# Performance work log

Hardware: AMD Instinct MI355X
Metric: run time of the kernel (lower is better)

## Reference

```python
import jax, jax.numpy as jnp
import numpy as np

B, H, W, DIM, WS, SHIFT, HEADS = 32, 56, 56, 256, 7, 3, 8
N = WS * WS          # 49 tokens per window
C2 = 2 * DIM         # concatenated two-modal channel dim
NW = (H // WS) * (W // WS)


def _rel_index(ws):
    coords = np.stack(np.meshgrid(np.arange(ws), np.arange(ws), indexing='ij')).reshape(2, -1)
    rel = (coords[:, :, None] - coords[:, None, :]).transpose(1, 2, 0)
    rel[:, :, 0] += ws - 1
    rel[:, :, 1] += ws - 1
    rel[:, :, 0] *= 2 * ws - 1
    return rel.sum(-1)  # (N, N) int

REL_IDX = _rel_index(WS).reshape(-1)


def _attn_mask():
    # standard Swin shifted-window mask: 0 / -100 per window pair
    img = np.zeros((H, W))
    cnt = 0
    for hs in (slice(0, H - WS), slice(H - WS, H - SHIFT), slice(H - SHIFT, H)):
        for ws_ in (slice(0, W - WS), slice(W - WS, W - SHIFT), slice(W - SHIFT, W)):
            img[hs, ws_] = cnt
            cnt += 1
    mw = img.reshape(H // WS, WS, W // WS, WS).transpose(0, 2, 1, 3).reshape(-1, N)
    d = mw[:, None, :] - mw[:, :, None]
    return np.where(d != 0, -100.0, 0.0).astype(np.float32)  # (nW, N, N)

ATTN_MASK = _attn_mask()


def _win_part(x):  # (B,H,W,C) -> (nW*B, N, C)
    b, c = x.shape[0], x.shape[-1]
    x = x.reshape(b, H // WS, WS, W // WS, WS, c).transpose(0, 1, 3, 2, 4, 5)
    return x.reshape(-1, N, c)


def _win_rev(w, b):  # (nW*B, N, C) -> (B,H,W,C)
    c = w.shape[-1]
    x = w.reshape(b, H // WS, W // WS, WS, WS, c).transpose(0, 1, 3, 2, 4, 5)
    return x.reshape(b, H, W, c)


def _ln(t, g, bb):
    m = t.mean(-1, keepdims=True)
    v = t.var(-1, keepdims=True)
    return (t - m) / jnp.sqrt(v + 1e-5) * g + bb


def setup_inputs() -> dict:
    key = jax.random.key(0)
    ks = jax.random.split(key, 8)
    def nrm(k, shape, s=0.02):
        return jax.random.normal(k, shape, jnp.float32) * s
    return {
        'x': jax.random.normal(ks[0], (B, H * W, DIM), jnp.float32),
        'y': jax.random.normal(ks[1], (B, H * W, DIM), jnp.float32),
        'g1': jnp.ones((DIM,), jnp.float32), 'b1': jnp.zeros((DIM,), jnp.float32),
        'rpb': nrm(ks[2], ((2 * WS - 1) * (2 * WS - 1), HEADS)),
        'w_qkv': nrm(ks[3], (6 * DIM, 2 * DIM)), 'b_qkv': jnp.zeros((6 * DIM,), jnp.float32),
        'w_proj': nrm(ks[4], (DIM, 2 * DIM)), 'b_proj': jnp.zeros((DIM,), jnp.float32),
        'g2': jnp.ones((DIM,), jnp.float32), 'b2': jnp.zeros((DIM,), jnp.float32),
        'w_fc1': nrm(ks[5], (4 * DIM, DIM)), 'b_fc1': jnp.zeros((4 * DIM,), jnp.float32),
        'w_fc2': nrm(ks[6], (DIM, 4 * DIM)), 'b_fc2': jnp.zeros((DIM,), jnp.float32),
    }


def reference(x, y, g1, b1, rpb, w_qkv, b_qkv, w_proj, b_proj, g2, b2, w_fc1, b_fc1, w_fc2, b_fc2):
    scale = (DIM // HEADS) ** -0.5  # as in __init__: head_dim = dim // num_heads
    shortcut = x
    xn = _ln(x, g1, b1).reshape(B, H, W, DIM)
    yn = _ln(y, g1, b1).reshape(B, H, W, DIM)
    # cyclic shift
    xn = jnp.roll(xn, (-SHIFT, -SHIFT), axis=(1, 2))
    yn = jnp.roll(yn, (-SHIFT, -SHIFT), axis=(1, 2))
    xw, yw = _win_part(xn), _win_part(yn)            # (nW*B, N, C)
    xy = jnp.concatenate([xw, yw], axis=-1)          # (nW*B, N, 2C)
    nwb, hd = xy.shape[0], C2 // HEADS
    qkv = (xy @ w_qkv.T + b_qkv).reshape(nwb, N, 3, HEADS, hd).transpose(2, 0, 3, 1, 4)
    q, k, v = qkv[0] * scale, qkv[1], qkv[2]         # (nW*B, h, N, d)
    attn = jnp.einsum('whnd,whmd->whnm', q, k)
    bias = rpb[REL_IDX].reshape(N, N, HEADS).transpose(2, 0, 1)  # (h, N, N)
    attn = attn + bias[None]
    attn = attn.reshape(B, NW, HEADS, N, N) + jnp.asarray(ATTN_MASK)[None, :, None]
    attn = jax.nn.softmax(attn.reshape(nwb, HEADS, N, N), axis=-1)
    out = jnp.einsum('whnm,whmd->whnd', attn, v).transpose(0, 2, 1, 3).reshape(nwb, N, C2)
    out = out @ w_proj.T + b_proj                    # fuse 2C -> C
    out = _win_rev(out, B)
    out = jnp.roll(out, (SHIFT, SHIFT), axis=(1, 2)).reshape(B, H * W, DIM)
    x = shortcut + out
    h = _ln(x, g2, b2)
    h = jax.nn.gelu(h @ w_fc1.T + b_fc1, approximate=False)
    return x + h @ w_fc2.T + b_fc2
```

## Files before the change

### kernel.cpp

```cpp
#include <hip/hip_runtime.h>
#include <hip/hip_bf16.h>

#define DEVI __device__ __forceinline__

typedef __attribute__((ext_vector_type(8))) short short8;
typedef __attribute__((ext_vector_type(4))) float f32x4;
typedef unsigned int u32;
typedef unsigned short u16;

typedef __attribute__((address_space(1))) const u32 gu32_t;
typedef __attribute__((address_space(3))) u32 lu32_t;

DEVI u16 f2bf(float f) {
  u32 u = __builtin_bit_cast(u32, f);
  u32 r = (u + 0x7fffu + ((u >> 16) & 1u)) >> 16;
  return (u16)r;
}

DEVI f32x4 mfma16(short8 a, short8 b, f32x4 c) {
  return __builtin_amdgcn_mfma_f32_16x16x32_bf16(a, b, c, 0, 0, 0);
}

DEVI void gload16(const void* g, void* l) {
  __builtin_amdgcn_global_load_lds((gu32_t*)g, (lu32_t*)l, 16, 0, 0);
}

#define CHUNK_ROWS 25088
#define PLANE ((size_t)CHUNK_ROWS * 64)
#define KOFF  ((size_t)8 * PLANE)
#define VOFF  ((size_t)16 * PLANE)

__global__ __launch_bounds__(256) void convk(const float* __restrict__ s, u16* __restrict__ d, int n4) {
  int i = blockIdx.x * 256 + threadIdx.x;
  if (i < n4) {
    const float4 v = ((const float4*)s)[i];
    ushort4 o;
    o.x = f2bf(v.x); o.y = f2bf(v.y); o.z = f2bf(v.z); o.w = f2bf(v.w);
    ((ushort4*)d)[i] = o;
  }
}

__global__ __launch_bounds__(256) void btab_build(const float* __restrict__ rpb, float* __restrict__ btab) {
  const int cls = blockIdx.x >> 3, h = blockIdx.x & 7;
  float* dst = btab + (size_t)(cls * 8 + h) * 4096;
  for (int e = threadIdx.x; e < 4096; e += 256) {
    const int n = e >> 6, m = e & 63;
    float v;
    if (m >= 49) {
      v = -1e30f;
    } else if (n >= 49) {
      v = 0.f;
    } else {
      const int r1 = n / 7, c1 = n - r1 * 7;
      const int r2 = m / 7, c2 = m - r2 * 7;
      const int rel = (r1 - r2 + 6) * 13 + (c1 - c2 + 6);
      v = rpb[rel * 8 + h];
      const int reg1 = ((cls & 1) ? (r1 < 4 ? 1 : 2) : 0) * 3 + ((cls & 2) ? (c1 < 4 ? 1 : 2) : 0);
      const int reg2 = ((cls & 1) ? (r2 < 4 ? 1 : 2) : 0) * 3 + ((cls & 2) ? (c2 < 4 ? 1 : 2) : 0);
      if (reg1 != reg2) v -= 100.f;
    }
    dst[e] = v;
  }
}

__global__ __launch_bounds__(256) void ln_gather(
    const float* __restrict__ x, const float* __restrict__ y,
    const float* __restrict__ g1, const float* __restrict__ b1,
    u16* __restrict__ XY, int rowbase)
{
  const int wv = threadIdx.x >> 6, lane = threadIdx.x & 63;
  const int rl = blockIdx.x * 4 + wv;
  const int row = rowbase + rl;
  const int w = row / 49, n = row - w * 49;
  const int b = w >> 6, win = w & 63, wh = win >> 3, ww = win & 7;
  const int r = n / 7, c = n - r * 7;
  int oh = wh * 7 + r + 3; if (oh >= 56) oh -= 56;
  int ow = ww * 7 + c + 3; if (ow >= 56) ow -= 56;
  const size_t po = ((size_t)b * 3136 + oh * 56 + ow) * 256;
  const float4 g1v = ((const float4*)g1)[lane];
  const float4 b1v = ((const float4*)b1)[lane];
  u16* orow = XY + (size_t)rl * 512;
  #pragma unroll
  for (int mod = 0; mod < 2; ++mod) {
    const float* src = (mod ? y : x) + po;
    const float4 v = ((const float4*)src)[lane];
    float s = v.x + v.y + v.z + v.w;
    #pragma unroll
    for (int off = 1; off < 64; off <<= 1) s += __shfl_xor(s, off);
    const float mean = s * (1.0f / 256.0f);
    const float d0 = v.x - mean, d1 = v.y - mean, d2 = v.z - mean, d3 = v.w - mean;
    float sq = d0 * d0 + d1 * d1 + d2 * d2 + d3 * d3;
    #pragma unroll
    for (int off = 1; off < 64; off <<= 1) sq += __shfl_xor(sq, off);
    const float rstd = rsqrtf(sq * (1.0f / 256.0f) + 1e-5f);
    ushort4 o;
    o.x = f2bf(d0 * rstd * g1v.x + b1v.x);
    o.y = f2bf(d1 * rstd * g1v.y + b1v.y);
    o.z = f2bf(d2 * rstd * g1v.z + b1v.z);
    o.w = f2bf(d3 * rstd * g1v.w + b1v.w);
    *(ushort4*)(orow + mod * 256 + lane * 4) = o;
  }
}

__global__ __launch_bounds__(256) void qkv_gemm(
    const u16* __restrict__ A, const u16* __restrict__ Bw,
    const float* __restrict__ bias, u16* __restrict__ Qo)
{
  __shared__ __align__(16) u16 sA[128 * 64];
  __shared__ __align__(16) u16 sB[128 * 64];
  const int nx = gridDim.x;
  const int nwg = nx * gridDim.y;
  const int orig = blockIdx.y * nx + blockIdx.x;
  const int sw = (orig & 7) * (nwg >> 3) + (orig >> 3);
  const int m0  = (sw / nx) * 128;
  const int nn0 = (sw % nx) * 128;
  const int tid = threadIdx.x;
  const int lane = tid & 63;
  const int wv = tid >> 6;
  const int wm = wv >> 1, wn = wv & 1;
  const int rq = lane & 15, kg = lane >> 4;
  f32x4 acc[4][4];
  #pragma unroll
  for (int i = 0; i < 4; ++i)
    #pragma unroll
    for (int j = 0; j < 4; ++j) acc[i][j] = f32x4{0,0,0,0};

  for (int kt = 0; kt < 8; ++kt) {
    if (kt) __syncthreads();
    #pragma unroll
    for (int i = 0; i < 4; ++i) {
      const int c = i * 256 + tid;
      gload16(A + (size_t)(m0 + (c >> 3)) * 512 + kt * 64 + (c & 7) * 8, sA + c * 8);
    }
    #pragma unroll
    for (int i = 0; i < 4; ++i) {
      const int c = i * 256 + tid;
      gload16(Bw + (size_t)(nn0 + (c >> 3)) * 512 + kt * 64 + (c & 7) * 8, sB + c * 8);
    }
    __syncthreads();
    #pragma unroll
    for (int k0 = 0; k0 < 2; ++k0) {
      short8 af[4], bf8[4];
      #pragma unroll
      for (int mt = 0; mt < 4; ++mt)
        af[mt] = *(const short8*)(sA + (wm * 64 + mt * 16 + rq) * 64 + k0 * 32 + kg * 8);
      #pragma unroll
      for (int nt = 0; nt < 4; ++nt)
        bf8[nt] = *(const short8*)(sB + (wn * 64 + nt * 16 + rq) * 64 + k0 * 32 + kg * 8);
      #pragma unroll
      for (int mt = 0; mt < 4; ++mt)
        #pragma unroll
        for (int nt = 0; nt < 4; ++nt)
          acc[mt][nt] = mfma16(af[mt], bf8[nt], acc[mt][nt]);
    }
  }
  #pragma unroll
  for (int mt = 0; mt < 4; ++mt) {
    #pragma unroll
    for (int nt = 0; nt < 4; ++nt) {
      const int col = nn0 + wn * 64 + nt * 16 + rq;
      const int t = col >> 9, rem = col & 511;
      const int h = rem >> 6, d = rem & 63;
      const float bc = bias[col];
      const float sc = (t == 0) ? 0.17677669529663687f : 1.0f;
      u16* bp = Qo + (size_t)(t * 8 + h) * PLANE + d;
      #pragma unroll
      for (int r = 0; r < 4; ++r) {
        const int row = m0 + wm * 64 + mt * 16 + kg * 4 + r;
        bp[(size_t)row * 64] = f2bf((acc[mt][nt][r] + bc) * sc);
      }
    }
  }
}

__global__ __launch_bounds__(256, 3) void attn3(
    const u16* __restrict__ qkv, const float* __restrict__ btab,
    u16* __restrict__ concat, int wbase)
{
  __shared__ __align__(16) u16 sP[4][3136];
  __shared__ __align__(16) u16 sVT[4][4608];

  const int tid = threadIdx.x;
  const int wv = tid >> 6, lane = tid & 63;
  const int rq = lane & 15, kg = lane >> 4;
  const int gw = blockIdx.x * 4 + wv;
  const int wl = gw >> 3, h = gw & 7;
  const int w = wbase + wl;
  const int win = w & 63, wh = win >> 3, ww = win & 7;
  const int cls = ((wh == 7) ? 1 : 0) | ((ww == 7) ? 2 : 0);
  const float* Tb = btab + (size_t)(cls * 8 + h) * 4096;
  u16* sPw = sP[wv];
  u16* sVw = sVT[wv];

  const u16* qbase = qkv + (size_t)h * PLANE + (size_t)wl * 49 * 64;
  const u16* kbase = qkv + KOFF + (size_t)h * PLANE + (size_t)wl * 49 * 64;
  const u16* vbase = qkv + VOFF + (size_t)h * PLANE + (size_t)wl * 49 * 64;

  short8 vreg[4][2];
  #pragma unroll
  for (int t = 0; t < 4; ++t)
    #pragma unroll
    for (int h2 = 0; h2 < 2; ++h2)
      vreg[t][h2] = *(const short8*)(vbase + (size_t)(16 * t + rq) * 64 + kg * 8 + h2 * 32);

  short8 ak[4][2];
  #pragma unroll
  for (int j = 0; j < 4; ++j) {
    const int rr = (16 * j + rq) > 48 ? 48 : (16 * j + rq);
    ak[j][0] = *(const short8*)(kbase + rr * 64 + kg * 8);
    ak[j][1] = *(const short8*)(kbase + rr * 64 + 32 + kg * 8);
  }
  f32x4 sacc[4][4];
  #pragma unroll
  for (int i = 0; i < 4; ++i)
    #pragma unroll
    for (int j = 0; j < 4; ++j) sacc[i][j] = f32x4{0,0,0,0};
  #pragma unroll
  for (int i = 0; i < 4; ++i) {
    const int rr = (16 * i + rq) > 48 ? 48 : (16 * i + rq);
    const short8 a0 = *(const short8*)(qbase + rr * 64 + kg * 8);
    const short8 a1 = *(const short8*)(qbase + rr * 64 + 32 + kg * 8);
    #pragma unroll
    for (int j = 0; j < 4; ++j) {
      sacc[i][j] = mfma16(a0, ak[j][0], sacc[i][j]);
      sacc[i][j] = mfma16(a1, ak[j][1], sacc[i][j]);
    }
  }

  #pragma unroll
  for (int t = 0; t < 4; ++t) {
    const int row = 16 * t + rq;
    #pragma unroll
    for (int h2 = 0; h2 < 2; ++h2) {
      const int c0 = kg * 8 + h2 * 32;
      #pragma unroll
      for (int j = 0; j < 8; ++j)
        sVw[(c0 + j) * 72 + (row ^ (kg << 4))] = (u16)vreg[t][h2][j];
    }
  }

  #pragma unroll
  for (int i = 0; i < 4; ++i) {
    #pragma unroll
    for (int r = 0; r < 4; ++r) {
      const int n = 16 * i + kg * 4 + r;
      const float* Trow = Tb + n * 64 + rq;
      float pv[4];
      #pragma unroll
      for (int j = 0; j < 4; ++j)
        pv[j] = sacc[i][j][r] + Trow[16 * j];
      float mx = fmaxf(fmaxf(pv[0], pv[1]), fmaxf(pv[2], pv[3]));
      #pragma unroll
      for (int off = 1; off < 16; off <<= 1) mx = fmaxf(mx, __shfl_xor(mx, off));
      float sm = 0.f;
      #pragma unroll
      for (int j = 0; j < 4; ++j) { const float e = __expf(pv[j] - mx); pv[j] = e; sm += e; }
      #pragma unroll
      for (int off = 1; off < 16; off <<= 1) sm += __shfl_xor(sm, off);
      const float inv = 1.0f / sm;
      if (n < 49) {
        #pragma unroll
        for (int j = 0; j < 4; ++j) {
          const int col = 16 * j + rq;
          sPw[n * 64 + (((col >> 3) ^ (n & 7)) << 3) + (col & 7)] = f2bf(pv[j] * inv);
        }
      }
    }
  }

  f32x4 oacc[4][4];
  #pragma unroll
  for (int i = 0; i < 4; ++i)
    #pragma unroll
    for (int j = 0; j < 4; ++j) oacc[i][j] = f32x4{0,0,0,0};
  #pragma unroll
  for (int m0v = 0; m0v < 2; ++m0v) {
    short8 av[4];
    #pragma unroll
    for (int ct = 0; ct < 4; ++ct) {
      const int col = ct * 16 + rq;
      const int s = (col >> 3) & 3;
      short8 vvv = *(const short8*)(sVw + col * 72 + ((m0v * 32 + kg * 8) ^ (s << 4)));
      if (m0v == 1) {
        if (kg == 3) {
          #pragma unroll
          for (int e = 0; e < 8; ++e) vvv[e] = 0;
        } else if (kg == 2) {
          #pragma unroll
          for (int e = 1; e < 8; ++e) vvv[e] = 0;
        }
      }
      av[ct] = vvv;
    }
    #pragma unroll
    for (int i = 0; i < 4; ++i) {
      const int rr = (16 * i + rq) > 48 ? 48 : (16 * i + rq);
      const int ch = (m0v * 4 + kg) ^ (rr & 7);
      const short8 pa = *(const short8*)(sPw + rr * 64 + ch * 8);
      #pragma unroll
      for (int ct = 0; ct < 4; ++ct)
        oacc[i][ct] = mfma16(pa, av[ct], oacc[i][ct]);
    }
  }

  __builtin_amdgcn_s_waitcnt(0);
  #pragma unroll
  for (int i = 0; i < 4; ++i)
    #pragma unroll
    for (int ct = 0; ct < 4; ++ct)
      #pragma unroll
      for (int r = 0; r < 4; ++r) {
        const int n = 16 * i + kg * 4 + r;
        if (n < 49) {
          const int col = ct * 16 + rq;
          sPw[n * 64 + (((col >> 3) ^ (n & 7)) << 3) + (col & 7)] = f2bf(oacc[i][ct][r]);
        }
      }
  u16* crow = concat + (size_t)(wl * 49) * 512 + h * 64;
  #pragma unroll
  for (int it = 0; it < 7; ++it) {
    const int c = it * 64 + lane;
    if (c < 392) {
      const int m = c >> 3, s = c & 7;
      const short8 vvv = *(const short8*)(sPw + m * 64 + ((s ^ (m & 7)) << 3));
      *(short8*)(crow + (size_t)m * 512 + s * 8) = vvv;
    }
  }
}

__global__ __launch_bounds__(256, 2) void projln(
    const u16* __restrict__ A, const u16* __restrict__ Bw,
    const float* __restrict__ bias, const float* __restrict__ x,
    const float* __restrict__ g2, const float* __restrict__ b2,
    float* __restrict__ out, u16* __restrict__ xn2, int rowbase)
{
  __shared__ __align__(16) u16 sA[128 * 64];
  __shared__ __align__(16) u16 sB[256 * 64];
  const int m0 = blockIdx.x * 128;
  const int tid = threadIdx.x;
  const int lane = tid & 63;
  const int wv = tid >> 6;
  const int rq = lane & 15, kg = lane >> 4;
  f32x4 acc[2][16];
  #pragma unroll
  for (int i = 0; i < 2; ++i)
    #pragma unroll
    for (int j = 0; j < 16; ++j) acc[i][j] = f32x4{0,0,0,0};

  for (int kt = 0; kt < 8; ++kt) {
    if (kt) __syncthreads();
    #pragma unroll
    for (int i = 0; i < 4; ++i) {
      const int c = i * 256 + tid;
      gload16(A + (size_t)(m0 + (c >> 3)) * 512 + kt * 64 + (c & 7) * 8, sA + c * 8);
    }
    #pragma unroll
    for (int i = 0; i < 8; ++i) {
      const int c = i * 256 + tid;
      gload16(Bw + (size_t)(c >> 3) * 512 + kt * 64 + (c & 7) * 8, sB + c * 8);
    }
    __syncthreads();
    #pragma unroll
    for (int k0 = 0; k0 < 2; ++k0) {
      short8 af[2];
      #pragma unroll
      for (int mt = 0; mt < 2; ++mt)
        af[mt] = *(const short8*)(sA + (wv * 32 + mt * 16 + rq) * 64 + k0 * 32 + kg * 8);
      #pragma unroll
      for (int nt = 0; nt < 16; ++nt) {
        const short8 bf8 = *(const short8*)(sB + (nt * 16 + rq) * 64 + k0 * 32 + kg * 8);
        #pragma unroll
        for (int mt = 0; mt < 2; ++mt)
          acc[mt][nt] = mfma16(af[mt], bf8, acc[mt][nt]);
      }
    }
  }

  float br[16], g2r[16], b2r[16];
  #pragma unroll
  for (int nt = 0; nt < 16; ++nt) {
    const int col = nt * 16 + rq;
    br[nt] = bias[col]; g2r[nt] = g2[col]; b2r[nt] = b2[col];
  }
  #pragma unroll
  for (int mt = 0; mt < 2; ++mt) {
    #pragma unroll
    for (int r = 0; r < 4; ++r) {
      const int row = m0 + wv * 32 + mt * 16 + kg * 4 + r;
      const u32 g = (u32)(rowbase + row);
      const u32 w = g / 49u; const u32 n = g - w * 49u;
      const int b = w >> 6, win = w & 63, wh = win >> 3, ww = win & 7;
      const u32 rr = n / 7u; const u32 cc = n - rr * 7u;
      int oh = wh * 7 + (int)rr + 3; if (oh >= 56) oh -= 56;
      int ow = ww * 7 + (int)cc + 3; if (ow >= 56) ow -= 56;
      const size_t po = ((size_t)b * 3136 + oh * 56 + ow) * 256;
      float vals[16];
      float s = 0.f;
      #pragma unroll
      for (int nt = 0; nt < 16; ++nt) {
        const float v = acc[mt][nt][r] + br[nt] + x[po + nt * 16 + rq];
        vals[nt] = v; s += v;
      }
      #pragma unroll
      for (int off = 1; off < 16; off <<= 1) s += __shfl_xor(s, off);
      const float mean = s * (1.0f / 256.0f);
      float sq = 0.f;
      #pragma unroll
      for (int nt = 0; nt < 16; ++nt) { const float d_ = vals[nt] - mean; sq += d_ * d_; }
      #pragma unroll
      for (int off = 1; off < 16; off <<= 1) sq += __shfl_xor(sq, off);
      const float rstd = rsqrtf(sq * (1.0f / 256.0f) + 1e-5f);
      #pragma unroll
      for (int nt = 0; nt < 16; ++nt) {
        const int col = nt * 16 + rq;
        out[po + col] = vals[nt];
        xn2[po + col] = f2bf((vals[nt] - mean) * rstd * g2r[nt] + b2r[nt]);
      }
    }
  }
}

template<int K, int NOUT, bool GELU>
__global__ __launch_bounds__(256) void mlp_gemm(
    const u16* __restrict__ A, const u16* __restrict__ Bw,
    const float* __restrict__ bias, u16* __restrict__ obf, float* __restrict__ ofr)
{
  __shared__ __align__(16) u16 sA[128 * 64];
  __shared__ __align__(16) u16 sB[128 * 64];
  const int nx = gridDim.x;
  const int nwg = nx * gridDim.y;
  const int orig = blockIdx.y * nx + blockIdx.x;
  const int sw = (orig & 7) * (nwg >> 3) + (orig >> 3);
  const int m0  = (sw / nx) * 128;
  const int nn0 = (sw % nx) * 128;
  const int tid = threadIdx.x;
  const int lane = tid & 63;
  const int wv = tid >> 6;
  const int wm = wv >> 1, wn = wv & 1;
  const int rq = lane & 15, kg = lane >> 4;
  f32x4 acc[4][4];
  #pragma unroll
  for (int i = 0; i < 4; ++i)
    #pragma unroll
    for (int j = 0; j < 4; ++j) acc[i][j] = f32x4{0,0,0,0};

  for (int kt = 0; kt < K / 64; ++kt) {
    if (kt) __syncthreads();
    #pragma unroll
    for (int i = 0; i < 4; ++i) {
      const int c = i * 256 + tid;
      gload16(A + (size_t)(m0 + (c >> 3)) * K + kt * 64 + (c & 7) * 8, sA + c * 8);
    }
    #pragma unroll
    for (int i = 0; i < 4; ++i) {
      const int c = i * 256 + tid;
      gload16(Bw + (size_t)(nn0 + (c >> 3)) * K + kt * 64 + (c & 7) * 8, sB + c * 8);
    }
    __syncthreads();
    #pragma unroll
    for (int k0 = 0; k0 < 2; ++k0) {
      short8 af[4], bf8[4];
      #pragma unroll
      for (int mt = 0; mt < 4; ++mt)
        af[mt] = *(const short8*)(sA + (wm * 64 + mt * 16 + rq) * 64 + k0 * 32 + kg * 8);
      #pragma unroll
      for (int nt = 0; nt < 4; ++nt)
        bf8[nt] = *(const short8*)(sB + (wn * 64 + nt * 16 + rq) * 64 + k0 * 32 + kg * 8);
      #pragma unroll
      for (int mt = 0; mt < 4; ++mt)
        #pragma unroll
        for (int nt = 0; nt < 4; ++nt)
          acc[mt][nt] = mfma16(af[mt], bf8[nt], acc[mt][nt]);
    }
  }
  #pragma unroll
  for (int mt = 0; mt < 4; ++mt) {
    #pragma unroll
    for (int nt = 0; nt < 4; ++nt) {
      const int col = nn0 + wn * 64 + nt * 16 + rq;
      const float bcol = bias[col];
      #pragma unroll
      for (int r = 0; r < 4; ++r) {
        const int row = m0 + wm * 64 + mt * 16 + kg * 4 + r;
        float v = acc[mt][nt][r] + bcol;
        if constexpr (GELU) {
          v = 0.5f * v * (1.0f + erff(v * 0.7071067811865476f));
          obf[(size_t)row * NOUT + col] = f2bf(v);
        } else {
          float* p = ofr + (size_t)row * NOUT + col;
          *p = v + *p;
        }
      }
    }
  }
}

extern "C" void kernel_launch(void* const* d_in, const int* in_sizes, int n_in,
                              void* d_out, int out_size, void* d_ws, size_t ws_size,
                              hipStream_t stream) {
  const float* x      = (const float*)d_in[0];
  const float* y      = (const float*)d_in[1];
  const float* g1     = (const float*)d_in[2];
  const float* b1     = (const float*)d_in[3];
  const float* rpb    = (const float*)d_in[4];
  const float* w_qkv  = (const float*)d_in[5];
  const float* b_qkv  = (const float*)d_in[6];
  const float* w_proj = (const float*)d_in[7];
  const float* b_proj = (const float*)d_in[8];
  const float* g2     = (const float*)d_in[9];
  const float* b2     = (const float*)d_in[10];
  const float* w_fc1  = (const float*)d_in[11];
  const float* b_fc1  = (const float*)d_in[12];
  const float* w_fc2  = (const float*)d_in[13];
  const float* b_fc2  = (const float*)d_in[14];
  float* out = (float*)d_out;

  u16* wsp = (u16*)d_ws;
  u16* wqkv_bf  = wsp;
  u16* wproj_bf = wsp + 786432;
  u16* wfc1_bf  = wsp + 917504;
  u16* wfc2_bf  = wsp + 1179648;
  float* btab   = (float*)(wsp + 1441792);
  u16* xn2      = wsp + 1703936;
  u16* XYc      = wsp + 27394048;
  u16* qkvc     = wsp + 40239104;
  u16* hbuf     = XYc;

  convk<<<768, 256, 0, stream>>>(w_qkv,  wqkv_bf,  196608);
  convk<<<128, 256, 0, stream>>>(w_proj, wproj_bf, 32768);
  convk<<<256, 256, 0, stream>>>(w_fc1,  wfc1_bf,  65536);
  convk<<<256, 256, 0, stream>>>(w_fc2,  wfc2_bf,  65536);
  btab_build<<<32, 256, 0, stream>>>(rpb, btab);

  for (int c = 0; c < 4; ++c) {
    ln_gather<<<6272, 256, 0, stream>>>(x, y, g1, b1, XYc, c * CHUNK_ROWS);
    qkv_gemm<<<dim3(12, 196), 256, 0, stream>>>(XYc, wqkv_bf, b_qkv, qkvc);
    attn3<<<1024, 256, 0, stream>>>(qkvc, btab, XYc, c * 512);
    projln<<<196, 256, 0, stream>>>(XYc, wproj_bf, b_proj, x, g2, b2, out, xn2, c * CHUNK_ROWS);
  }

  for (int c = 0; c < 2; ++c) {
    mlp_gemm<256, 1024, true><<<dim3(8, 392), 256, 0, stream>>>(
        xn2 + (size_t)c * 50176 * 256, wfc1_bf, b_fc1, hbuf, nullptr);
    mlp_gemm<1024, 256, false><<<dim3(2, 392), 256, 0, stream>>>(
        hbuf, wfc2_bf, b_fc2, nullptr, out + (size_t)c * 50176 * 256);
  }
}
```

Before: 964.6 us.

## Fuse MLP fc1, GELU and fc2 into one kernel with the hidden tile kept in LDS

Replaces the two chunked MLP GEMM launches with a single kernel. Each block takes 64 rows, stages the LayerNorm output in XOR-swizzled LDS, and builds the hidden layer 128 columns at a time. Each hidden slice goes through GELU into LDS and is immediately accumulated into the fc2 result, so the 1024-wide hidden activation is never written to or read back from global memory. Weight fragments are read straight from global memory/cache rather than staged in LDS, which may cost bandwidth. The exact erf GELU is also replaced with a tanh approximation using __expf, which slightly changes the numerics relative to the reference.

Result: faster. 866.2 us (-10.2%).

```diff
diff --git a/kernel.cpp b/kernel.cpp
--- a/kernel.cpp
+++ b/kernel.cpp
@@ -23,6 +23,12 @@
 
 DEVI void gload16(const void* g, void* l) {
   __builtin_amdgcn_global_load_lds((gu32_t*)g, (lu32_t*)l, 16, 0, 0);
+}
+
+DEVI float gelu_t(float v) {
+  const float u = v * (0.7978845608f + 0.0356774081f * v * v);
+  const float t = 1.0f - 2.0f / (__expf(2.0f * u) + 1.0f);
+  return 0.5f * v * (1.0f + t);
 }
 
 #define CHUNK_ROWS 25088
@@ -420,78 +426,102 @@
   }
 }
 
-template<int K, int NOUT, bool GELU>
-__global__ __launch_bounds__(256) void mlp_gemm(
-    const u16* __restrict__ A, const u16* __restrict__ Bw,
-    const float* __restrict__ bias, u16* __restrict__ obf, float* __restrict__ ofr)
+__global__ __launch_bounds__(256, 3) void fused_mlp(
+    const u16* __restrict__ xn2, const u16* __restrict__ w1,
+    const float* __restrict__ bf1, const u16* __restrict__ w2,
+    const float* __restrict__ bf2v, float* __restrict__ out)
 {
-  __shared__ __align__(16) u16 sA[128 * 64];
-  __shared__ __align__(16) u16 sB[128 * 64];
-  const int nx = gridDim.x;
-  const int nwg = nx * gridDim.y;
-  const int orig = blockIdx.y * nx + blockIdx.x;
-  const int sw = (orig & 7) * (nwg >> 3) + (orig >> 3);
-  const int m0  = (sw / nx) * 128;
-  const int nn0 = (sw % nx) * 128;
+  __shared__ __align__(16) u16 sX[64 * 256];
+  __shared__ __align__(16) u16 sH[64 * 128];
+
+  const int m0 = blockIdx.x * 64;
   const int tid = threadIdx.x;
-  const int lane = tid & 63;
-  const int wv = tid >> 6;
-  const int wm = wv >> 1, wn = wv & 1;
+  const int wv = tid >> 6, lane = tid & 63;
   const int rq = lane & 15, kg = lane >> 4;
-  f32x4 acc[4][4];
+
+  #pragma unroll
+  for (int i = 0; i < 8; ++i) {
+    const int c = i * 256 + tid;
+    const int row = c >> 5, ch = c & 31;
+    const int sch = (ch & 24) | ((ch ^ row) & 7);
+    gload16(xn2 + (size_t)(m0 + row) * 256 + sch * 8, sX + c * 8);
+  }
+
+  f32x4 acc2[4][4];
   #pragma unroll
   for (int i = 0; i < 4; ++i)
     #pragma unroll
-    for (int j = 0; j < 4; ++j) acc[i][j] = f32x4{0,0,0,0};
-
-  for (int kt = 0; kt < K / 64; ++kt) {
-    if (kt) __syncthreads();
-    #pragma unroll
-    for (int i = 0; i < 4; ++i) {
-      const int c = i * 256 + tid;
-      gload16(A + (size_t)(m0 + (c >> 3)) * K + kt * 64 + (c & 7) * 8, sA + c * 8);
-    }
-    #pragma unroll
-    for (int i = 0; i < 4; ++i) {
-      const int c = i * 256 + tid;
-      gload16(Bw + (size_t)(nn0 + (c >> 3)) * K + kt * 64 + (c & 7) * 8, sB + c * 8);
+    for (int j = 0; j < 4; ++j) acc2[i][j] = f32x4{0,0,0,0};
+
+  __syncthreads();
+
+  for (int t = 0; t < 8; ++t) {
+    f32x4 a1[4][2];
+    #pragma unroll
+    for (int i = 0; i < 4; ++i)
+      #pragma unroll
+      for (int j = 0; j < 2; ++j) a1[i][j] = f32x4{0,0,0,0};
+    #pragma unroll
+    for (int ks = 0; ks < 8; ++ks) {
+      short8 bfr[2];
+      #pragma unroll
+      for (int nt = 0; nt < 2; ++nt)
+        bfr[nt] = *(const short8*)(w1 + (size_t)(t * 128 + wv * 32 + nt * 16 + rq) * 256 + ks * 32 + kg * 8);
+      #pragma unroll
+      for (int mt = 0; mt < 4; ++mt) {
+        const int R = mt * 16 + rq;
+        const int wk = ks * 4 + kg;
+        const short8 af = *(const short8*)(sX + R * 256 + ((wk & 24) | ((wk ^ R) & 7)) * 8);
+        #pragma unroll
+        for (int nt = 0; nt < 2; ++nt)
+          a1[mt][nt] = mfma16(af, bfr[nt], a1[mt][nt]);
+      }
     }
     __syncthreads();
     #pragma unroll
-    for (int k0 = 0; k0 < 2; ++k0) {
-      short8 af[4], bf8[4];
-      #pragma unroll
-      for (int mt = 0; mt < 4; ++mt)
-        af[mt] = *(const short8*)(sA + (wm * 64 + mt * 16 + rq) * 64 + k0 * 32 + kg * 8);
-      #pragma unroll
-      for (int nt = 0; nt < 4; ++nt)
-        bf8[nt] = *(const short8*)(sB + (wn * 64 + nt * 16 + rq) * 64 + k0 * 32 + kg * 8);
+    for (int nt = 0; nt < 2; ++nt) {
+      const int col = wv * 32 + nt * 16 + rq;
+      const float bb = bf1[t * 128 + col];
+      const int ch = col >> 3;
       #pragma unroll
       for (int mt = 0; mt < 4; ++mt)
         #pragma unroll
+        for (int r = 0; r < 4; ++r) {
+          const int row = mt * 16 + kg * 4 + r;
+          sH[row * 128 + ((ch & 8) | ((ch ^ row) & 7)) * 8 + (col & 7)] =
+              f2bf(gelu_t(a1[mt][nt][r] + bb));
+        }
+    }
+    __syncthreads();
+    #pragma unroll
+    for (int ks = 0; ks < 4; ++ks) {
+      short8 bfr2[4];
+      #pragma unroll
+      for (int nt = 0; nt < 4; ++nt)
+        bfr2[nt] = *(const short8*)(w2 + (size_t)(wv * 64 + nt * 16 + rq) * 1024 + t * 128 + ks * 32 + kg * 8);
+      #pragma unroll
+      for (int mt = 0; mt < 4; ++mt) {
+        const int R = mt * 16 + rq;
+        const int wk = ks * 4 + kg;
+        const short8 af = *(const short8*)(sH + R * 128 + ((wk & 8) | ((wk ^ R) & 7)) * 8);
+        #pragma unroll
         for (int nt = 0; nt < 4; ++nt)
-          acc[mt][nt] = mfma16(af[mt], bf8[nt], acc[mt][nt]);
-    }
-  }
-  #pragma unroll
-  for (int mt = 0; mt < 4; ++mt) {
-    #pragma unroll
-    for (int nt = 0; nt < 4; ++nt) {
-      const int col = nn0 + wn * 64 + nt * 16 + rq;
-      const float bcol = bias[col];
+          acc2[mt][nt] = mfma16(af, bfr2[nt], acc2[mt][nt]);
+      }
+    }
+  }
+
+  #pragma unroll
+  for (int nt = 0; nt < 4; ++nt) {
+    const int col = wv * 64 + nt * 16 + rq;
+    const float bb = bf2v[col];
+    #pragma unroll
+    for (int mt = 0; mt < 4; ++mt)
       #pragma unroll
       for (int r = 0; r < 4; ++r) {
-        const int row = m0 + wm * 64 + mt * 16 + kg * 4 + r;
-        float v = acc[mt][nt][r] + bcol;
-        if constexpr (GELU) {
-          v = 0.5f * v * (1.0f + erff(v * 0.7071067811865476f));
-          obf[(size_t)row * NOUT + col] = f2bf(v);
-        } else {
-          float* p = ofr + (size_t)row * NOUT + col;
-          *p = v + *p;
-        }
-      }
-    }
+        float* p = out + (size_t)(m0 + mt * 16 + kg * 4 + r) * 256 + col;
+        *p = acc2[mt][nt][r] + bb + *p;
+      }
   }
 }
 
@@ -524,7 +554,6 @@
   u16* xn2      = wsp + 1703936;
   u16* XYc      = wsp + 27394048;
   u16* qkvc     = wsp + 40239104;
-  u16* hbuf     = XYc;
 
   convk<<<768, 256, 0, stream>>>(w_qkv,  wqkv_bf,  196608);
   convk<<<128, 256, 0, stream>>>(w_proj, wproj_bf, 32768);
@@ -539,10 +568,5 @@
     projln<<<196, 256, 0, stream>>>(XYc, wproj_bf, b_proj, x, g2, b2, out, xn2, c * CHUNK_ROWS);
   }
 
-  for (int c = 0; c < 2; ++c) {
-    mlp_gemm<256, 1024, true><<<dim3(8, 392), 256, 0, stream>>>(
-        xn2 + (size_t)c * 50176 * 256, wfc1_bf, b_fc1, hbuf, nullptr);
-    mlp_gemm<1024, 256, false><<<dim3(2, 392), 256, 0, stream>>>(
-        hbuf, wfc2_bf, b_fc2, nullptr, out + (size_t)c * 50176 * 256);
-  }
-}
+  fused_mlp<<<1568, 256, 0, stream>>>(xn2, wfc1_bf, b_fc1, wfc2_bf, b_fc2, out);
+}
```
